# Kernel optimization log

Measured on AMD Instinct MI355X. Metric: run time of the kernel, lower is better.

Reference implementation:

```python
import jax, jax.numpy as jnp
import numpy as np

N = 10000   # nodes
E = 50000   # edges
G = 8       # graphs in batch
IN = 16     # input_dim
H = 64      # hidden_dim
EH = 32     # edge-network hidden
L = 3       # num ECC layers
BN_EPS = 1e-5


def _xavier(k, shape):
    fan_in, fan_out = shape[-2], shape[-1]
    s = jnp.sqrt(2.0 / (fan_in + fan_out)).astype(jnp.float32)
    return jax.random.normal(k, shape, jnp.float32) * s


def setup_inputs() -> dict:
    key = jax.random.key(0)
    ks = jax.random.split(key, 10)
    x = jax.random.normal(ks[0], (N, IN), jnp.float32)
    edge_index = jax.random.randint(ks[1], (2, E), 0, N, jnp.int32)
    batch = jnp.sort(jax.random.randint(ks[2], (N,), 0, G, jnp.int32))
    return {
        "x": x,
        "edge_index": edge_index,
        "batch": batch,
        "emb_w": _xavier(ks[3], (IN, H)),
        "emb_b": jnp.zeros((H,), jnp.float32),
        "e1_w": _xavier(ks[4], (L, 1, EH)),
        "e1_b": jnp.zeros((L, EH), jnp.float32),
        "e2_w": _xavier(ks[5], (L, EH, H * H)),
        "e2_b": jnp.zeros((L, H * H), jnp.float32),
        "self_w": _xavier(ks[6], (L, H, H)),
        "self_b": jnp.zeros((L, H), jnp.float32),
        "bn_g": jnp.ones((L, H), jnp.float32),
        "bn_b": jnp.zeros((L, H), jnp.float32),
        "cls_w": _xavier(ks[7], (2 * H, 1)),
        "cls_b": jnp.zeros((1,), jnp.float32),
    }


def reference(x, edge_index, batch, emb_w, emb_b, e1_w, e1_b, e2_w, e2_b,
              self_w, self_b, bn_g, bn_b, cls_w, cls_b):
    src, dst = edge_index[0], edge_index[1]
    # in-degree of targets for 'mean' aggregation (computed once; edge structure fixed)
    deg = jnp.clip(jax.ops.segment_sum(jnp.ones((E,), x.dtype), dst, num_segments=N), 1.0, None)

    h = x @ emb_w + emb_b  # [N, H] input embedding
    for l in range(L):
        # edge_attr: L2 distance between first 3 hidden channels of endpoints, [E,1]
        d = h[src, :3] - h[dst, :3]
        ea = jnp.sqrt(jnp.sum(d * d, axis=1, keepdims=True))
        # edge network -> per-edge dynamic weight matrix [E, H, H]
        hid = jax.nn.relu(ea @ e1_w[l] + e1_b[l])          # [E, EH]
        W = (hid @ e2_w[l] + e2_b[l]).reshape(E, H, H)
        # message: x_j (source features) times per-edge weight
        msg = jnp.einsum('ei,eio->eo', h[src], W)          # [E, H]
        agg = jax.ops.segment_sum(msg, dst, num_segments=N) / deg[:, None]
        h2 = agg + h @ self_w[l] + self_b[l]               # ECC output + self transform
        # BatchNorm1d (training-mode batch stats, biased variance), then ReLU
        mu = h2.mean(axis=0)
        var = h2.var(axis=0)
        h = jax.nn.relu(bn_g[l] * (h2 - mu) * jax.lax.rsqrt(var + BN_EPS) + bn_b[l])
        # dropout is a no-op in eval mode

    cnt = jnp.clip(jax.ops.segment_sum(jnp.ones((N,), h.dtype), batch, num_segments=G), 1.0, None)
    h_mean = jax.ops.segment_sum(h, batch, num_segments=G) / cnt[:, None]
    h_max = jax.ops.segment_max(h, batch, num_segments=G)
    h_pooled = jnp.concatenate([h_mean, h_max], axis=1)    # [G, 2H]
    return jax.nn.sigmoid(h_pooled @ cls_w + cls_b)        # [G, 1]
```

## Files before the change

### kernel.cpp

```cpp
#include <hip/hip_runtime.h>
#include <math.h>

#define N_NODES 10000
#define N_EDGES 50000
#define N_GRAPHS 8
#define IN_DIM  16
#define HID     64
#define EHID    32
#define NLAYER  3
#define NK      33
#define BN_EPS  1e-5f
#define POOL_BLOCKS 63
#define LAYER_BLOCKS 625

#define OFF_H0     0u
#define OFF_H2A    640000u
#define OFF_H2B    1280000u
#define OFF_ATAB   1920000u
#define OFF_CTAB   2325504u
#define OFF_S      2731008u
#define OFF_NB     2731136u
#define OFF_DEG    2731200u
#define OFF_ROWPTR 2741200u
#define OFF_CUR    2751248u
#define OFF_CSRC   2761248u
#define OFF_STATS  2811248u
#define OFF_GSUM   2811632u
#define OFF_GMAX   2812144u
#define OFF_GCNT   2812656u
#define OFF_CNTR   2812664u

__device__ __forceinline__ float rl(float v, int i) {
    return __int_as_float(__builtin_amdgcn_readlane(__float_as_int(v), i));
}

__device__ __forceinline__ void bn_coef(const float* __restrict__ sPrev,
                                        const float* __restrict__ gPrev,
                                        const float* __restrict__ bPrev,
                                        int c, float& sc, float& sf) {
    float mu  = sPrev[c] * (1.0f / N_NODES);
    float var = fmaf(-mu, mu, sPrev[64 + c] * (1.0f / N_NODES));
    float rstd = 1.0f / sqrtf(var + BN_EPS);
    sc = gPrev[c] * rstd;
    sf = fmaf(-sc, mu, bPrev[c]);
}

__global__ void k_prep(const float* __restrict__ e1w, const float* __restrict__ e1b,
                       float* __restrict__ s_arr, int* __restrict__ nb,
                       int* __restrict__ deg, int* __restrict__ cur,
                       float* __restrict__ stats,
                       float* __restrict__ gsum, float* __restrict__ gmax,
                       int* __restrict__ gcnt, int* __restrict__ counter) {
    int l = blockIdx.x;
    if (threadIdx.x == 0) {
        float t[EHID]; int c = 0;
        for (int j = 0; j < EHID; ++j) {
            float a = e1w[l * EHID + j], b = e1b[l * EHID + j];
            if ((a > 0.f && b < 0.f) || (a < 0.f && b > 0.f)) t[c++] = -b / a;
        }
        for (int i = 1; i < c; ++i) {
            float v = t[i]; int j = i - 1;
            while (j >= 0 && t[j] > v) { t[j + 1] = t[j]; --j; }
            t[j + 1] = v;
        }
        nb[l] = c;
        for (int i = 0; i < c; ++i) s_arr[l * NK + i] = t[i];
    }
    if (l == 0) {
        for (int i = threadIdx.x; i < N_NODES; i += 256) { deg[i] = 0; cur[i] = 0; }
    } else if (l == 1) {
        for (int i = threadIdx.x; i < N_GRAPHS * HID; i += 256) { gsum[i] = 0.f; gmax[i] = 0.f; }
        if (threadIdx.x < N_GRAPHS) gcnt[threadIdx.x] = 0;
        if (threadIdx.x == 0) *counter = 0;
    } else {
        for (int i = threadIdx.x; i < NLAYER * 128; i += 256) stats[i] = 0.f;
    }
}

__global__ void k_deg(const int* __restrict__ ei, int* __restrict__ deg) {
    int e = blockIdx.x * blockDim.x + threadIdx.x;
    if (e < N_EDGES) atomicAdd(&deg[ei[N_EDGES + e]], 1);
}

__global__ void k_scan(const int* __restrict__ deg, int* __restrict__ rowptr) {
    __shared__ int part[256];
    int t = threadIdx.x;
    int base = t * 40;
    int s = 0;
    for (int i = 0; i < 40; ++i) {
        int n = base + i;
        if (n < N_NODES) s += deg[n];
    }
    part[t] = s;
    __syncthreads();
    for (int off = 1; off < 256; off <<= 1) {
        int v = (t >= off) ? part[t - off] : 0;
        __syncthreads();
        part[t] += v;
        __syncthreads();
    }
    int run = (t == 0) ? 0 : part[t - 1];
    for (int i = 0; i < 40; ++i) {
        int n = base + i;
        if (n < N_NODES) { rowptr[n] = run; run += deg[n]; }
    }
    if (t == 255) rowptr[N_NODES] = part[255];
}

__global__ void k_fill(const int* __restrict__ ei, const int* __restrict__ rowptr,
                       int* __restrict__ cur, int* __restrict__ csrc) {
    int e = blockIdx.x * blockDim.x + threadIdx.x;
    if (e < N_EDGES) {
        int dst = ei[N_EDGES + e];
        int pos = rowptr[dst] + atomicAdd(&cur[dst], 1);
        csrc[pos] = ei[e];
    }
}

__global__ void k_s2(const float* __restrict__ e1w, const float* __restrict__ e1b,
                     const float* __restrict__ e2w, const float* __restrict__ e2b,
                     const float* __restrict__ s_arr, const int* __restrict__ nb,
                     float* __restrict__ Atab, float* __restrict__ Ctab) {
    int q = blockIdx.x, k = blockIdx.y, l = blockIdx.z;
    int nbl = nb[l];
    if (k > nbl) return;
    __shared__ float sma[EHID], smb[EHID];
    if (threadIdx.x < EHID) {
        float a = e1w[l * EHID + threadIdx.x], b = e1b[l * EHID + threadIdx.x];
        float lo = (k == 0) ? 0.f : s_arr[l * NK + k - 1];
        float hi = s_arr[l * NK + k];
        float p  = (k == nbl) ? (lo + 1.0f) : 0.5f * (lo + hi);
        float m  = (p * a + b > 0.f) ? 1.f : 0.f;
        sma[threadIdx.x] = m * a;
        smb[threadIdx.x] = m * b;
    }
    __syncthreads();
    int f4 = q * 64 + threadIdx.x;
    const float4* w4base = (const float4*)(e2w);
    float4 accA = make_float4(0.f, 0.f, 0.f, 0.f);
    float4 accC = ((const float4*)(e2b + l * HID * HID))[f4];
    #pragma unroll
    for (int j = 0; j < EHID; ++j) {
        float4 w = w4base[(l * EHID + j) * 1024 + f4];
        float ma = sma[j], mb = smb[j];
        accA.x = fmaf(ma, w.x, accA.x); accA.y = fmaf(ma, w.y, accA.y);
        accA.z = fmaf(ma, w.z, accA.z); accA.w = fmaf(ma, w.w, accA.w);
        accC.x = fmaf(mb, w.x, accC.x); accC.y = fmaf(mb, w.y, accC.y);
        accC.z = fmaf(mb, w.z, accC.z); accC.w = fmaf(mb, w.w, accC.w);
    }
    ((float4*)(Atab + (l * NK + k) * (HID * HID)))[f4] = accA;
    ((float4*)(Ctab + (l * NK + k) * (HID * HID)))[f4] = accC;
}

__global__ void k_embed(const float* __restrict__ x, const float* __restrict__ w,
                        const float* __restrict__ b, float* __restrict__ h0) {
    int idx = blockIdx.x * blockDim.x + threadIdx.x;
    int n = idx >> 6, o = idx & 63;
    const float* xr = x + n * IN_DIM;
    float acc = b[o];
    #pragma unroll
    for (int i = 0; i < IN_DIM; ++i) acc = fmaf(xr[i], w[i * HID + o], acc);
    h0[idx] = acc;
}

__global__ void __launch_bounds__(256, 2)
k_layer(const float* __restrict__ hb, int useBN,
        const float* __restrict__ sPrev, const float* __restrict__ gPrev,
        const float* __restrict__ bPrev,
        const int* __restrict__ rowptr, const int* __restrict__ csrc,
        const int* __restrict__ deg,
        const float* __restrict__ Atab, const float* __restrict__ Ctab,
        const float* __restrict__ s_arr, const int* __restrict__ nbp, int l,
        const float* __restrict__ sw_l, const float* __restrict__ sb_l,
        float* __restrict__ h2out, float* __restrict__ statsOut) {
    __shared__ float smW[3 * HID * HID];
    __shared__ float sRed[2][4][HID];
    int tid = threadIdx.x, wid = tid >> 6, lane = tid & 63;
    int nb = nbp[l];
    const float* A0 = Atab + l * NK * HID * HID;
    const float* C0 = Ctab + l * NK * HID * HID;
    {
        float4* s4 = (float4*)smW;
        const float4* w4 = (const float4*)sw_l;
        const float4* a4 = (const float4*)A0;
        const float4* c4 = (const float4*)C0;
        #pragma unroll
        for (int p = 0; p < 4; ++p) {
            int j = p * 256 + tid;
            s4[j] = w4[j];
            s4[1024 + j] = a4[j];
            s4[2048 + j] = c4[j];
        }
    }
    __syncthreads();
    float sc = 0.f, sf = 0.f;
    if (useBN) bn_coef(sPrev, gPrev, bPrev, lane, sc, sf);
    float sbv = sb_l[lane];
    int nodeBase = blockIdx.x * 16 + wid * 4;

    float hvv[4], pp[4], qq[4], aggE[4];
    #pragma unroll
    for (int c = 0; c < 4; ++c) {
        int node = nodeBase + c;
        float hv = hb[node * HID + lane];
        if (useBN) hv = fmaxf(fmaf(sc, hv, sf), 0.f);
        hvv[c] = hv;
        float p = 0.f, q = 0.f, aggv = 0.f;
        int jb = rowptr[node], je = rowptr[node + 1];
        if (nb == 0) {
            int j = jb;
            for (; j + 4 <= je; j += 4) {
                int s0 = csrc[j], s1 = csrc[j + 1], s2 = csrc[j + 2], s3 = csrc[j + 3];
                float h0 = hb[s0 * HID + lane];
                float h1 = hb[s1 * HID + lane];
                float h2 = hb[s2 * HID + lane];
                float h3 = hb[s3 * HID + lane];
                #pragma unroll
                for (int u = 0; u < 4; ++u) {
                    float hs = (u == 0) ? h0 : (u == 1) ? h1 : (u == 2) ? h2 : h3;
                    if (useBN) hs = fmaxf(fmaf(sc, hs, sf), 0.f);
                    float diff = hs - hv;
                    float d0 = rl(diff, 0), d1 = rl(diff, 1), d2 = rl(diff, 2);
                    float ea = sqrtf(fmaf(d0, d0, fmaf(d1, d1, d2 * d2)));
                    p = fmaf(ea, hs, p);
                    q += hs;
                }
            }
            for (; j < je; ++j) {
                int s = csrc[j];
                float hs = hb[s * HID + lane];
                if (useBN) hs = fmaxf(fmaf(sc, hs, sf), 0.f);
                float diff = hs - hv;
                float d0 = rl(diff, 0), d1 = rl(diff, 1), d2 = rl(diff, 2);
                float ea = sqrtf(fmaf(d0, d0, fmaf(d1, d1, d2 * d2)));
                p = fmaf(ea, hs, p);
                q += hs;
            }
        } else {
            for (int j = jb; j < je; ++j) {
                int src = csrc[j];
                float hs = hb[src * HID + lane];
                if (useBN) hs = fmaxf(fmaf(sc, hs, sf), 0.f);
                float diff = hs - hv;
                float d0 = rl(diff, 0), d1 = rl(diff, 1), d2 = rl(diff, 2);
                float ea = sqrtf(fmaf(d0, d0, fmaf(d1, d1, d2 * d2)));
                int k = 0;
                for (int i = 0; i < nb; ++i) k += (ea > s_arr[l * NK + i]) ? 1 : 0;
                const float* A = Atab + (l * NK + k) * (HID * HID);
                const float* C = Ctab + (l * NK + k) * (HID * HID);
                float au = 0.f, cu = 0.f;
                for (int i = 0; i < HID; ++i) {
                    float hi = rl(hs, i);
                    au = fmaf(hi, A[i * HID + lane], au);
                    cu = fmaf(hi, C[i * HID + lane], cu);
                }
                aggv += fmaf(ea, au, cu);
            }
        }
        pp[c] = p; qq[c] = q; aggE[c] = aggv;
    }

    float acc[4], agg[4];
    #pragma unroll
    for (int c = 0; c < 4; ++c) { acc[c] = sbv; agg[c] = 0.f; }
    #pragma unroll
    for (int i = 0; i < HID; ++i) {
        float ws = smW[i * HID + lane];
        float wa = smW[HID * HID + i * HID + lane];
        float wc = smW[2 * HID * HID + i * HID + lane];
        #pragma unroll
        for (int c = 0; c < 4; ++c) {
            acc[c] = fmaf(rl(hvv[c], i), ws, acc[c]);
            agg[c] = fmaf(rl(pp[c], i), wa, agg[c]);
            agg[c] = fmaf(rl(qq[c], i), wc, agg[c]);
        }
    }

    float ls = 0.f, ls2 = 0.f;
    #pragma unroll
    for (int c = 0; c < 4; ++c) {
        int node = nodeBase + c;
        float invd = 1.0f / fmaxf((float)deg[node], 1.0f);
        float v = fmaf(agg[c] + aggE[c], invd, acc[c]);
        h2out[node * HID + lane] = v;
        ls += v; ls2 = fmaf(v, v, ls2);
    }
    sRed[0][wid][lane] = ls;
    sRed[1][wid][lane] = ls2;
    __syncthreads();
    if (tid < HID) {
        float s  = sRed[0][0][tid] + sRed[0][1][tid] + sRed[0][2][tid] + sRed[0][3][tid];
        float s2 = sRed[1][0][tid] + sRed[1][1][tid] + sRed[1][2][tid] + sRed[1][3][tid];
        atomicAdd(&statsOut[tid], s);
        atomicAdd(&statsOut[64 + tid], s2);
    }
}

__global__ void k_bnpool(const float* __restrict__ h2cur, const float* __restrict__ s2,
                         const float* __restrict__ g2, const float* __restrict__ b2,
                         const int* __restrict__ batch,
                         float* __restrict__ gsum, float* __restrict__ gmax,
                         int* __restrict__ gcnt, int* __restrict__ counter,
                         const float* __restrict__ cw, const float* __restrict__ cb,
                         float* __restrict__ out) {
    int tid = threadIdx.x;
    int wid = (blockIdx.x * 256 + tid) >> 6, lane = tid & 63;
    float sc, sf; bn_coef(s2, g2, b2, lane, sc, sf);
    int n0 = wid * 40;
    int n1 = min(n0 + 40, N_NODES);
    float asum = 0.f, amax = 0.f;
    int cb2 = -1, run = 0;
    for (int n = n0; n < n1; ++n) {
        int b = batch[n];
        float v = fmaxf(fmaf(sc, h2cur[n * HID + lane], sf), 0.f);
        if (b != cb2) {
            if (cb2 >= 0) {
                atomicAdd(&gsum[cb2 * HID + lane], asum);
                atomicMax((int*)&gmax[cb2 * HID + lane], __float_as_int(amax));
                if (lane == 0) atomicAdd(&gcnt[cb2], run);
            }
            cb2 = b; asum = v; amax = v; run = 1;
        } else {
            asum += v; amax = fmaxf(amax, v); ++run;
        }
    }
    if (cb2 >= 0) {
        atomicAdd(&gsum[cb2 * HID + lane], asum);
        atomicMax((int*)&gmax[cb2 * HID + lane], __float_as_int(amax));
        if (lane == 0) atomicAdd(&gcnt[cb2], run);
    }
    __threadfence();
    __shared__ int lastFlag;
    if (tid == 0) {
        int old = __hip_atomic_fetch_add(counter, 1, __ATOMIC_ACQ_REL, __HIP_MEMORY_SCOPE_AGENT);
        lastFlag = (old == POOL_BLOCKS - 1);
    }
    __syncthreads();
    if (lastFlag && tid < N_GRAPHS) {
        int g = tid;
        float cnt = fmaxf((float)__hip_atomic_load(&gcnt[g], __ATOMIC_RELAXED, __HIP_MEMORY_SCOPE_AGENT), 1.f);
        float acc = cb[0];
        for (int o2 = 0; o2 < HID; ++o2) {
            float sv = __hip_atomic_load(&gsum[g * HID + o2], __ATOMIC_RELAXED, __HIP_MEMORY_SCOPE_AGENT);
            acc = fmaf(sv / cnt, cw[o2], acc);
        }
        for (int o2 = 0; o2 < HID; ++o2) {
            int iv = __hip_atomic_load((int*)&gmax[g * HID + o2], __ATOMIC_RELAXED, __HIP_MEMORY_SCOPE_AGENT);
            acc = fmaf(__int_as_float(iv), cw[HID + o2], acc);
        }
        out[g] = 1.0f / (1.0f + expf(-acc));
    }
}

extern "C" void kernel_launch(void* const* d_in, const int* in_sizes, int n_in,
                              void* d_out, int out_size, void* d_ws, size_t ws_size,
                              hipStream_t stream) {
    const float* x      = (const float*)d_in[0];
    const int*   ei     = (const int*)  d_in[1];
    const int*   batch  = (const int*)  d_in[2];
    const float* emb_w  = (const float*)d_in[3];
    const float* emb_b  = (const float*)d_in[4];
    const float* e1_w   = (const float*)d_in[5];
    const float* e1_b   = (const float*)d_in[6];
    const float* e2_w   = (const float*)d_in[7];
    const float* e2_b   = (const float*)d_in[8];
    const float* self_w = (const float*)d_in[9];
    const float* self_b = (const float*)d_in[10];
    const float* bn_g   = (const float*)d_in[11];
    const float* bn_b   = (const float*)d_in[12];
    const float* cls_w  = (const float*)d_in[13];
    const float* cls_b  = (const float*)d_in[14];
    float* out = (float*)d_out;

    float* wsf = (float*)d_ws;
    float* h0     = wsf + OFF_H0;
    float* h2a    = wsf + OFF_H2A;
    float* h2b    = wsf + OFF_H2B;
    float* Atab   = wsf + OFF_ATAB;
    float* Ctab   = wsf + OFF_CTAB;
    float* s_arr  = wsf + OFF_S;
    int*   nb     = (int*)(wsf + OFF_NB);
    int*   deg    = (int*)(wsf + OFF_DEG);
    int*   rowptr = (int*)(wsf + OFF_ROWPTR);
    int*   cur    = (int*)(wsf + OFF_CUR);
    int*   csrc   = (int*)(wsf + OFF_CSRC);
    float* stats  = wsf + OFF_STATS;
    float* gsum   = wsf + OFF_GSUM;
    float* gmax   = wsf + OFF_GMAX;
    int*   gcnt   = (int*)(wsf + OFF_GCNT);
    int*   cntr   = (int*)(wsf + OFF_CNTR);

    k_prep<<<NLAYER, 256, 0, stream>>>(e1_w, e1_b, s_arr, nb, deg, cur, stats, gsum, gmax, gcnt, cntr);
    k_deg<<<(N_EDGES + 255) / 256, 256, 0, stream>>>(ei, deg);
    k_scan<<<1, 256, 0, stream>>>(deg, rowptr);
    k_fill<<<(N_EDGES + 255) / 256, 256, 0, stream>>>(ei, rowptr, cur, csrc);
    k_s2<<<dim3(16, NK, NLAYER), 64, 0, stream>>>(e1_w, e1_b, e2_w, e2_b, s_arr, nb, Atab, Ctab);
    k_embed<<<(N_NODES * HID) / 256, 256, 0, stream>>>(x, emb_w, emb_b, h0);

    for (int l = 0; l < NLAYER; ++l) {
        const float* hb    = (l == 0) ? h0 : ((l == 1) ? h2a : h2b);
        float*       h2out = (l == 1) ? h2b : h2a;
        const float* sPrev = stats + (l - 1) * 128;
        const float* gPrev = bn_g + (l - 1) * HID;
        const float* bPrev = bn_b + (l - 1) * HID;
        int useBN = (l > 0);
        k_layer<<<LAYER_BLOCKS, 256, 0, stream>>>(hb, useBN, sPrev, gPrev, bPrev,
                                                  rowptr, csrc, deg,
                                                  Atab, Ctab, s_arr, nb, l,
                                                  self_w + l * HID * HID, self_b + l * HID,
                                                  h2out, stats + l * 128);
    }

    k_bnpool<<<POOL_BLOCKS, 256, 0, stream>>>(h2a, stats + 2 * 128, bn_g + 2 * HID, bn_b + 2 * HID,
                                              batch, gsum, gmax, gcnt, cntr, cls_w, cls_b, out);
}
```

Before: 173.4 us.

## Fuse whole pipeline into one cooperative persistent kernel with grid syncs

Result: slower. 461.8 us (+166.4%).

```diff
diff --git a/kernel.cpp b/kernel.cpp
--- a/kernel.cpp
+++ b/kernel.cpp
@@ -1,5 +1,8 @@
 #include <hip/hip_runtime.h>
+#include <hip/hip_cooperative_groups.h>
 #include <math.h>
+
+namespace cg = cooperative_groups;
 
 #define N_NODES 10000
 #define N_EDGES 50000
@@ -10,6 +13,8 @@
 #define NLAYER  3
 #define NK      33
 #define BN_EPS  1e-5f
+#define GRID_BLKS 256
+#define NTHREADS 256
 #define POOL_BLOCKS 63
 #define LAYER_BLOCKS 625
 
@@ -43,6 +48,319 @@
     float rstd = 1.0f / sqrtf(var + BN_EPS);
     sc = gPrev[c] * rstd;
     sf = fmaf(-sc, mu, bPrev[c]);
+}
+
+__global__ void __launch_bounds__(NTHREADS, 2)
+k_mega(const float* __restrict__ x, const int* __restrict__ ei,
+       const int* __restrict__ batch,
+       const float* __restrict__ emb_w, const float* __restrict__ emb_b,
+       const float* __restrict__ e1w, const float* __restrict__ e1b,
+       const float* __restrict__ e2w, const float* __restrict__ e2b,
+       const float* __restrict__ self_w, const float* __restrict__ self_b,
+       const float* __restrict__ bn_g, const float* __restrict__ bn_b,
+       const float* __restrict__ cls_w, const float* __restrict__ cls_b,
+       float* __restrict__ wsf, float* __restrict__ out)
+{
+    cg::grid_group grid = cg::this_grid();
+    __shared__ float smW[3 * HID * HID];
+    __shared__ float sRed[2][4][HID];
+    __shared__ float sma[EHID], smb[EHID];
+
+    float* h0     = wsf + OFF_H0;
+    float* h2a    = wsf + OFF_H2A;
+    float* h2b    = wsf + OFF_H2B;
+    float* Atab   = wsf + OFF_ATAB;
+    float* Ctab   = wsf + OFF_CTAB;
+    float* s_arr  = wsf + OFF_S;
+    int*   nbp    = (int*)(wsf + OFF_NB);
+    int*   deg    = (int*)(wsf + OFF_DEG);
+    int*   rowptr = (int*)(wsf + OFF_ROWPTR);
+    int*   cur    = (int*)(wsf + OFF_CUR);
+    int*   csrc   = (int*)(wsf + OFF_CSRC);
+    float* stats  = wsf + OFF_STATS;
+    float* gsum   = wsf + OFF_GSUM;
+    float* gmax   = wsf + OFF_GMAX;
+    int*   gcnt   = (int*)(wsf + OFF_GCNT);
+    int*   cntr   = (int*)(wsf + OFF_CNTR);
+
+    const int tid = threadIdx.x, bid = blockIdx.x;
+    const int wid = tid >> 6, lane = tid & 63;
+    const int gt = bid * NTHREADS + tid;
+    const int GT = GRID_BLKS * NTHREADS;
+
+    if (gt < N_NODES) { deg[gt] = 0; cur[gt] = 0; }
+    if (gt < NLAYER * 128) stats[gt] = 0.f;
+    if (gt < N_GRAPHS * HID) { gsum[gt] = 0.f; gmax[gt] = 0.f; }
+    if (gt < N_GRAPHS) gcnt[gt] = 0;
+    if (gt == 0) *cntr = 0;
+    if (gt < NLAYER) {
+        int l = gt;
+        float t[EHID]; int c = 0;
+        for (int j = 0; j < EHID; ++j) {
+            float a = e1w[l * EHID + j], b = e1b[l * EHID + j];
+            if ((a > 0.f && b < 0.f) || (a < 0.f && b > 0.f)) t[c++] = -b / a;
+        }
+        for (int i = 1; i < c; ++i) {
+            float v = t[i]; int j = i - 1;
+            while (j >= 0 && t[j] > v) { t[j + 1] = t[j]; --j; }
+            t[j + 1] = v;
+        }
+        nbp[l] = c;
+        for (int i = 0; i < c; ++i) s_arr[l * NK + i] = t[i];
+    }
+    for (int idx = gt; idx < N_NODES * HID; idx += GT) {
+        int n = idx >> 6, o = idx & 63;
+        const float* xr = x + n * IN_DIM;
+        float acc = emb_b[o];
+        #pragma unroll
+        for (int i = 0; i < IN_DIM; ++i) acc = fmaf(xr[i], emb_w[i * HID + o], acc);
+        h0[idx] = acc;
+    }
+    grid.sync();
+
+    for (int e = gt; e < N_EDGES; e += GT) atomicAdd(&deg[ei[N_EDGES + e]], 1);
+    if (bid < NK * NLAYER) {
+        int l = bid / NK, k = bid % NK;
+        int nbl = nbp[l];
+        if (k <= nbl) {
+            if (tid < EHID) {
+                float a = e1w[l * EHID + tid], b = e1b[l * EHID + tid];
+                float lo = (k == 0) ? 0.f : s_arr[l * NK + k - 1];
+                float hi = s_arr[l * NK + k];
+                float p  = (k == nbl) ? (lo + 1.0f) : 0.5f * (lo + hi);
+                float m  = (p * a + b > 0.f) ? 1.f : 0.f;
+                sma[tid] = m * a;
+                smb[tid] = m * b;
+            }
+            __syncthreads();
+            const float4* w4 = (const float4*)e2w;
+            #pragma unroll
+            for (int q = 0; q < 4; ++q) {
+                int f4 = q * 256 + tid;
+                float4 accA = make_float4(0.f, 0.f, 0.f, 0.f);
+                float4 accC = ((const float4*)(e2b + l * HID * HID))[f4];
+                #pragma unroll
+                for (int j = 0; j < EHID; ++j) {
+                    float4 w = w4[(l * EHID + j) * 1024 + f4];
+                    float ma = sma[j], mb = smb[j];
+                    accA.x = fmaf(ma, w.x, accA.x); accA.y = fmaf(ma, w.y, accA.y);
+                    accA.z = fmaf(ma, w.z, accA.z); accA.w = fmaf(ma, w.w, accA.w);
+                    accC.x = fmaf(mb, w.x, accC.x); accC.y = fmaf(mb, w.y, accC.y);
+                    accC.z = fmaf(mb, w.z, accC.z); accC.w = fmaf(mb, w.w, accC.w);
+                }
+                ((float4*)(Atab + (l * NK + k) * (HID * HID)))[f4] = accA;
+                ((float4*)(Ctab + (l * NK + k) * (HID * HID)))[f4] = accC;
+            }
+        }
+    }
+    grid.sync();
+
+    if (bid == 0) {
+        int* part = (int*)&sRed[0][0][0];
+        int base = tid * 40, s = 0;
+        for (int i = 0; i < 40; ++i) { int n = base + i; if (n < N_NODES) s += deg[n]; }
+        part[tid] = s;
+        __syncthreads();
+        for (int off = 1; off < 256; off <<= 1) {
+            int v = (tid >= off) ? part[tid - off] : 0;
+            __syncthreads();
+            part[tid] += v;
+            __syncthreads();
+        }
+        int run = (tid == 0) ? 0 : part[tid - 1];
+        for (int i = 0; i < 40; ++i) {
+            int n = base + i;
+            if (n < N_NODES) { rowptr[n] = run; run += deg[n]; }
+        }
+        if (tid == 255) rowptr[N_NODES] = part[255];
+    }
+    grid.sync();
+
+    for (int e = gt; e < N_EDGES; e += GT) {
+        int dst = ei[N_EDGES + e];
+        int pos = rowptr[dst] + atomicAdd(&cur[dst], 1);
+        csrc[pos] = ei[e];
+    }
+    grid.sync();
+
+    for (int l = 0; l < NLAYER; ++l) {
+        const float* hb    = (l == 0) ? h0 : ((l == 1) ? h2a : h2b);
+        float*       h2out = (l == 1) ? h2b : h2a;
+        const float* A0 = Atab + l * NK * HID * HID;
+        const float* C0 = Ctab + l * NK * HID * HID;
+        const float* swl = self_w + l * HID * HID;
+        int nbl = nbp[l];
+        {
+            float4* s4 = (float4*)smW;
+            const float4* w4 = (const float4*)swl;
+            const float4* a4 = (const float4*)A0;
+            const float4* c4 = (const float4*)C0;
+            #pragma unroll
+            for (int p2 = 0; p2 < 4; ++p2) {
+                int j = p2 * 256 + tid;
+                s4[j] = w4[j];
+                s4[1024 + j] = a4[j];
+                s4[2048 + j] = c4[j];
+            }
+        }
+        __syncthreads();
+        float sc = 0.f, sf = 0.f;
+        if (l > 0) bn_coef(stats + (l - 1) * 128, bn_g + (l - 1) * HID, bn_b + (l - 1) * HID, lane, sc, sf);
+        float sbv = self_b[l * HID + lane];
+        float ls = 0.f, ls2 = 0.f;
+
+        for (int c2 = 0; c2 < 2; ++c2) {
+            int nodeBase = bid * 40 + c2 * 20 + wid * 5;
+            float hvv[5], pp[5], qq[5], aggE[5];
+            #pragma unroll
+            for (int c = 0; c < 5; ++c) {
+                int node = nodeBase + c;
+                float hv = 0.f, p = 0.f, q = 0.f, av = 0.f;
+                if (node < N_NODES) {
+                    hv = hb[node * HID + lane];
+                    if (l > 0) hv = fmaxf(fmaf(sc, hv, sf), 0.f);
+                    int jb = rowptr[node], je = rowptr[node + 1];
+                    if (nbl == 0) {
+                        int j = jb;
+                        for (; j + 4 <= je; j += 4) {
+                            int s0 = csrc[j], s1 = csrc[j + 1], s2 = csrc[j + 2], s3 = csrc[j + 3];
+                            float g0 = hb[s0 * HID + lane];
+                            float g1 = hb[s1 * HID + lane];
+                            float g2 = hb[s2 * HID + lane];
+                            float g3 = hb[s3 * HID + lane];
+                            #pragma unroll
+                            for (int u = 0; u < 4; ++u) {
+                                float hs = (u == 0) ? g0 : (u == 1) ? g1 : (u == 2) ? g2 : g3;
+                                if (l > 0) hs = fmaxf(fmaf(sc, hs, sf), 0.f);
+                                float diff = hs - hv;
+                                float d0 = rl(diff, 0), d1 = rl(diff, 1), d2 = rl(diff, 2);
+                                float ea = sqrtf(fmaf(d0, d0, fmaf(d1, d1, d2 * d2)));
+                                p = fmaf(ea, hs, p);
+                                q += hs;
+                            }
+                        }
+                        for (; j < je; ++j) {
+                            int s = csrc[j];
+                            float hs = hb[s * HID + lane];
+                            if (l > 0) hs = fmaxf(fmaf(sc, hs, sf), 0.f);
+                            float diff = hs - hv;
+                            float d0 = rl(diff, 0), d1 = rl(diff, 1), d2 = rl(diff, 2);
+                            float ea = sqrtf(fmaf(d0, d0, fmaf(d1, d1, d2 * d2)));
+                            p = fmaf(ea, hs, p);
+                            q += hs;
+                        }
+                    } else {
+                        for (int j = jb; j < je; ++j) {
+                            int src = csrc[j];
+                            float hs = hb[src * HID + lane];
+                            if (l > 0) hs = fmaxf(fmaf(sc, hs, sf), 0.f);
+                            float diff = hs - hv;
+                            float d0 = rl(diff, 0), d1 = rl(diff, 1), d2 = rl(diff, 2);
+                            float ea = sqrtf(fmaf(d0, d0, fmaf(d1, d1, d2 * d2)));
+                            int k = 0;
+                            for (int i = 0; i < nbl; ++i) k += (ea > s_arr[l * NK + i]) ? 1 : 0;
+                            const float* A = Atab + (l * NK + k) * (HID * HID);
+                            const float* C = Ctab + (l * NK + k) * (HID * HID);
+                            float au = 0.f, cu = 0.f;
+                            for (int i = 0; i < HID; ++i) {
+                                float hi = rl(hs, i);
+                                au = fmaf(hi, A[i * HID + lane], au);
+                                cu = fmaf(hi, C[i * HID + lane], cu);
+                            }
+                            av += fmaf(ea, au, cu);
+                        }
+                    }
+                }
+                hvv[c] = hv; pp[c] = p; qq[c] = q; aggE[c] = av;
+            }
+
+            float acc[5], agg[5];
+            #pragma unroll
+            for (int c = 0; c < 5; ++c) { acc[c] = sbv; agg[c] = 0.f; }
+            #pragma unroll
+            for (int i = 0; i < HID; ++i) {
+                float ws = smW[i * HID + lane];
+                float wa = smW[HID * HID + i * HID + lane];
+                float wc = smW[2 * HID * HID + i * HID + lane];
+                #pragma unroll
+                for (int c = 0; c < 5; ++c) {
+                    acc[c] = fmaf(rl(hvv[c], i), ws, acc[c]);
+                    agg[c] = fmaf(rl(pp[c], i), wa, agg[c]);
+                    agg[c] = fmaf(rl(qq[c], i), wc, agg[c]);
+                }
+            }
+            #pragma unroll
+            for (int c = 0; c < 5; ++c) {
+                int node = nodeBase + c;
+                if (node < N_NODES) {
+                    float invd = 1.0f / fmaxf((float)deg[node], 1.0f);
+                    float v = fmaf(agg[c] + aggE[c], invd, acc[c]);
+                    h2out[node * HID + lane] = v;
+                    ls += v; ls2 = fmaf(v, v, ls2);
+                }
+            }
+        }
+        __syncthreads();
+        sRed[0][wid][lane] = ls;
+        sRed[1][wid][lane] = ls2;
+        __syncthreads();
+        if (tid < HID) {
+            float s  = sRed[0][0][tid] + sRed[0][1][tid] + sRed[0][2][tid] + sRed[0][3][tid];
+            float s2 = sRed[1][0][tid] + sRed[1][1][tid] + sRed[1][2][tid] + sRed[1][3][tid];
+            atomicAdd(&stats[l * 128 + tid], s);
+            atomicAdd(&stats[l * 128 + 64 + tid], s2);
+        }
+        grid.sync();
+    }
+
+    if (bid < POOL_BLOCKS) {
+        float sc, sf; bn_coef(stats + 2 * 128, bn_g + 2 * HID, bn_b + 2 * HID, lane, sc, sf);
+        int w = bid * 4 + wid;
+        int n0 = w * 40;
+        int n1 = min(n0 + 40, N_NODES);
+        float asum = 0.f, amax = 0.f;
+        int cb2 = -1, run = 0;
+        for (int n = n0; n < n1; ++n) {
+            int b = batch[n];
+            float v = fmaxf(fmaf(sc, h2a[n * HID + lane], sf), 0.f);
+            if (b != cb2) {
+                if (cb2 >= 0) {
+                    atomicAdd(&gsum[cb2 * HID + lane], asum);
+                    atomicMax((int*)&gmax[cb2 * HID + lane], __float_as_int(amax));
+                    if (lane == 0) atomicAdd(&gcnt[cb2], run);
+                }
+                cb2 = b; asum = v; amax = v; run = 1;
+            } else {
+                asum += v; amax = fmaxf(amax, v); ++run;
+            }
+        }
+        if (cb2 >= 0) {
+            atomicAdd(&gsum[cb2 * HID + lane], asum);
+            atomicMax((int*)&gmax[cb2 * HID + lane], __float_as_int(amax));
+            if (lane == 0) atomicAdd(&gcnt[cb2], run);
+        }
+        __threadfence();
+        __shared__ int lastFlag;
+        if (tid == 0) {
+            int old = __hip_atomic_fetch_add(cntr, 1, __ATOMIC_ACQ_REL, __HIP_MEMORY_SCOPE_AGENT);
+            lastFlag = (old == POOL_BLOCKS - 1);
+        }
+        __syncthreads();
+        if (lastFlag && tid < N_GRAPHS) {
+            int g = tid;
+            float cnt = fmaxf((float)__hip_atomic_load(&gcnt[g], __ATOMIC_RELAXED, __HIP_MEMORY_SCOPE_AGENT), 1.f);
+            float acc = cls_b[0];
+            for (int o2 = 0; o2 < HID; ++o2) {
+                float sv = __hip_atomic_load(&gsum[g * HID + o2], __ATOMIC_RELAXED, __HIP_MEMORY_SCOPE_AGENT);
+                acc = fmaf(sv / cnt, cls_w[o2], acc);
+            }
+            for (int o2 = 0; o2 < HID; ++o2) {
+                int iv = __hip_atomic_load((int*)&gmax[g * HID + o2], __ATOMIC_RELAXED, __HIP_MEMORY_SCOPE_AGENT);
+                acc = fmaf(__int_as_float(iv), cls_w[HID + o2], acc);
+            }
+            out[g] = 1.0f / (1.0f + expf(-acc));
+        }
+    }
 }
 
 __global__ void k_prep(const float* __restrict__ e1w, const float* __restrict__ e1b,
@@ -370,9 +688,20 @@
     const float* bn_b   = (const float*)d_in[12];
     const float* cls_w  = (const float*)d_in[13];
     const float* cls_b  = (const float*)d_in[14];
-    float* out = (float*)d_out;
-
     float* wsf = (float*)d_ws;
+    float* outp = (float*)d_out;
+
+    void* args[] = { (void*)&x, (void*)&ei, (void*)&batch,
+                     (void*)&emb_w, (void*)&emb_b,
+                     (void*)&e1_w, (void*)&e1_b, (void*)&e2_w, (void*)&e2_b,
+                     (void*)&self_w, (void*)&self_b,
+                     (void*)&bn_g, (void*)&bn_b,
+                     (void*)&cls_w, (void*)&cls_b,
+                     (void*)&wsf, (void*)&outp };
+    hipError_t err = hipLaunchCooperativeKernel((void*)k_mega, dim3(GRID_BLKS),
+                                                dim3(NTHREADS), args, 0, stream);
+    if (err == hipSuccess) return;
+
     float* h0     = wsf + OFF_H0;
     float* h2a    = wsf + OFF_H2A;
     float* h2b    = wsf + OFF_H2B;
@@ -412,5 +741,5 @@
     }
 
     k_bnpool<<<POOL_BLOCKS, 256, 0, stream>>>(h2a, stats + 2 * 128, bn_g + 2 * HID, bn_b + 2 * HID,
-                                              batch, gsum, gmax, gcnt, cntr, cls_w, cls_b, out);
-}
+                                              batch, gsum, gmax, gcnt, cntr, cls_w, cls_b, outp);
+}
```
